# Optimization experiments

Measured on AMD Instinct MI355X. Metric: run time of the kernel, lower is better.

Reference implementation:

```python
import jax, jax.numpy as jnp
import numpy as np

HEADS = 4
DIM_HEAD = 32
DIM = HEADS * DIM_HEAD  # 128
B, H, W, C = 32, 64, 64, 128
LN_EPS = 1e-5


def setup_inputs() -> dict:
    key = jax.random.key(0)
    k0, k1, k2, k3, k4 = jax.random.split(key, 5)
    x = jax.random.normal(k0, (B, H, W, C), dtype=jnp.float32)
    # 1x1 convs are pointwise dense layers over channels
    w_qkv = jax.random.normal(k1, (C, DIM * 3), dtype=jnp.float32) * (1.0 / np.sqrt(C))
    w_out = jax.random.normal(k2, (DIM, C), dtype=jnp.float32) * (1.0 / np.sqrt(DIM))
    b_out = jax.random.normal(k3, (C,), dtype=jnp.float32) * 0.01
    ln_scale = jnp.ones((C,), dtype=jnp.float32)
    return {"x": x, "w_qkv": w_qkv, "w_out": w_out, "b_out": b_out, "ln_scale": ln_scale}


def reference(x, w_qkv, w_out, b_out, ln_scale):
    b, h, w, c = x.shape
    n = h * w
    # qkv projection (1x1 conv, no bias)
    qkv = jnp.einsum('bhwc,cf->bhwf', x, w_qkv)  # [B,H,W,3*DIM]
    q, k, v = jnp.split(qkv, 3, axis=-1)
    # rearrange 'b x y (h d) -> b (x y) h d'
    q = q.reshape(b, n, HEADS, DIM_HEAD)
    k = k.reshape(b, n, HEADS, DIM_HEAD)
    v = v.reshape(b, n, HEADS, DIM_HEAD)
    q = jax.nn.softmax(q, axis=-1) * (1.0 / np.sqrt(DIM_HEAD))
    k = jax.nn.softmax(k, axis=1)  # softmax over spatial positions
    v = v * (1.0 / n)
    # per-head context: [B, heads, d, e]
    context = jnp.einsum('bnhd,bnhe->bhde', k, v)
    # out: 'b h d e, b n h d -> b h e n', then rearrange 'b h e (x y) -> b x y (h e)'
    out = jnp.einsum('bhde,bnhd->bnhe', context, q)  # [B, n, heads, e]
    out = out.reshape(b, h, w, DIM)  # channel order = (h e), matching rearrange
    # output 1x1 conv (with bias)
    out = jnp.einsum('bhwd,dc->bhwc', out, w_out) + b_out
    # LayerNorm over channels, eps=1e-5, no bias
    mu = jnp.mean(out, axis=-1, keepdims=True)
    var = jnp.mean(jnp.square(out - mu), axis=-1, keepdims=True)
    out = (out - mu) * jax.lax.rsqrt(var + LN_EPS) * ln_scale
    return out
```

## Files before the change

### kernel.cpp

```cpp
#include <hip/hip_runtime.h>
#include <hip/hip_bf16.h>

typedef __attribute__((ext_vector_type(4))) float f32x4;
typedef __attribute__((ext_vector_type(8))) short bf16x8;
typedef __attribute__((ext_vector_type(8))) unsigned short u16x8;

#define OFF_QS    0ull
#define OFF_EK    33554432ull
#define OFF_VV    67108864ull
#define OFF_PCTX  100663296ull
#define OFF_PSE   109051904ull
#define OFF_CTXG  109314048ull
#define OFF_WQT   109576192ull
#define OFF_WOT   109674496ull

static __device__ __forceinline__ unsigned short f2bf(float f) {
  unsigned int u = __builtin_bit_cast(unsigned int, f);
  return (unsigned short)((u + 0x7fffu + ((u >> 16) & 1u)) >> 16);
}
static __device__ __forceinline__ float bf2f(unsigned short v) {
  return __builtin_bit_cast(float, (unsigned int)v << 16);
}

__global__ __launch_bounds__(256) void k_prep(const float* __restrict__ wqkv,
                                              const float* __restrict__ wout,
                                              unsigned short* __restrict__ wqT,
                                              unsigned short* __restrict__ woT) {
  int idx = blockIdx.x * 256 + threadIdx.x;
  if (idx < 49152) {
    int f = idx >> 7, k = idx & 127;
    wqT[idx] = f2bf(wqkv[k * 384 + f]);
  } else {
    int j = idx - 49152;
    int c = j >> 7, k = j & 127;
    woT[j] = f2bf(wout[k * 128 + c]);
  }
}

__global__ __launch_bounds__(512, 4) void k_qkv(const float* __restrict__ x,
                                                const unsigned short* __restrict__ wqT,
                                                unsigned short* __restrict__ qs,
                                                unsigned short* __restrict__ ekh,
                                                unsigned short* __restrict__ vvh) {
  extern __shared__ char lds[];
  char* lds_w = lds;
  char* lds_a = lds + 32768;

  const int tid = threadIdx.x;
  const int tile = blockIdx.x;
  const int sec = blockIdx.y;
  const long rowbase = (long)tile * 128;

  {
    const int4* src = (const int4*)wqT + sec * 2048;
#pragma unroll
    for (int i = 0; i < 4; i++) {
      int u = tid + i * 512;
      ((int4*)lds_w)[u ^ ((u >> 4) & 7)] = src[u];
    }
  }
  {
    const f32x4* src = (const f32x4*)(x + rowbase * 128);
#pragma unroll
    for (int i = 0; i < 8; i++) {
      int u = tid + i * 512;
      f32x4 val = src[u];
      ushort4 bq;
      bq.x = f2bf(val.x); bq.y = f2bf(val.y); bq.z = f2bf(val.z); bq.w = f2bf(val.w);
      int ba = (u * 8) ^ (((u >> 5) & 7) << 4);
      *(ushort4*)(lds_a + ba) = bq;
    }
  }
  __syncthreads();

  const int lane = tid & 63, g = lane >> 4, c = lane & 15;
  const int wave = tid >> 6;
  const int wm = wave >> 2, wf = wave & 3;

  f32x4 acc[4][2];
#pragma unroll
  for (int mt = 0; mt < 4; mt++) { acc[mt][0] = (f32x4){0.f,0.f,0.f,0.f}; acc[mt][1] = (f32x4){0.f,0.f,0.f,0.f}; }

#pragma unroll
  for (int kk = 0; kk < 4; kk++) {
    const int koff = (kk * 32 + g * 8) * 2;
    bf16x8 af[4], bfrag[2];
#pragma unroll
    for (int mt = 0; mt < 4; mt++) {
      int row = wm * 64 + mt * 16 + c;
      af[mt] = *(const bf16x8*)(lds_a + ((row * 256 + koff) ^ ((row & 7) << 4)));
    }
#pragma unroll
    for (int ft = 0; ft < 2; ft++) {
      int frow = wf * 32 + ft * 16 + c;
      bfrag[ft] = *(const bf16x8*)(lds_w + ((frow * 256 + koff) ^ ((frow & 7) << 4)));
    }
#pragma unroll
    for (int mt = 0; mt < 4; mt++)
#pragma unroll
      for (int ft = 0; ft < 2; ft++)
        acc[mt][ft] = __builtin_amdgcn_mfma_f32_16x16x32_bf16(af[mt], bfrag[ft], acc[mt][ft], 0, 0, 0);
  }
  __syncthreads();

  const float RS32 = 0.17677669529663687f;
  const int sc = wf * 32;
#pragma unroll
  for (int mt = 0; mt < 4; mt++) {
    f32x4 a0 = acc[mt][0], a1 = acc[mt][1];
    int row0 = wm * 64 + mt * 16 + g * 4;
    if (sec == 0) {
#pragma unroll
      for (int r = 0; r < 4; r++) {
        float e0 = __expf(a0[r]), e1 = __expf(a1[r]);
        float s = e0 + e1;
        s += __shfl_xor(s, 1); s += __shfl_xor(s, 2);
        s += __shfl_xor(s, 4); s += __shfl_xor(s, 8);
        float inv = RS32 / s;
        int row = row0 + r;
        *(unsigned short*)(lds + ((row * 256 + (sc + c) * 2)      ^ ((row & 7) << 4))) = f2bf(e0 * inv);
        *(unsigned short*)(lds + ((row * 256 + (sc + c + 16) * 2) ^ ((row & 7) << 4))) = f2bf(e1 * inv);
      }
    } else if (sec == 1) {
#pragma unroll
      for (int r = 0; r < 4; r++) {
        int row = row0 + r;
        *(unsigned short*)(lds + ((row * 256 + (sc + c) * 2)      ^ ((row & 7) << 4))) = f2bf(__expf(a0[r]));
        *(unsigned short*)(lds + ((row * 256 + (sc + c + 16) * 2) ^ ((row & 7) << 4))) = f2bf(__expf(a1[r]));
      }
    } else {
#pragma unroll
      for (int r = 0; r < 4; r++) {
        int row = row0 + r;
        *(unsigned short*)(lds + ((row * 256 + (sc + c) * 2)      ^ ((row & 7) << 4))) = f2bf(a0[r]);
        *(unsigned short*)(lds + ((row * 256 + (sc + c + 16) * 2) ^ ((row & 7) << 4))) = f2bf(a1[r]);
      }
    }
  }
  __syncthreads();

  if (sec == 0) {
    const long off16 = (long)tile * 2048;
#pragma unroll
    for (int i = 0; i < 4; i++) {
      int u = tid + i * 512;
      int row = u >> 4;
      int4 v = *(const int4*)(lds + ((u * 16) ^ ((row & 7) << 4)));
      ((int4*)qs)[off16 + u] = v;
    }
  } else {
    unsigned short* dsth = (sec == 1) ? ekh : vvh;
#pragma unroll
    for (int i = 0; i < 4; i++) {
      int u = tid + i * 512;
      int row = u >> 4, col16 = u & 15;
      int h = col16 >> 2, q4 = col16 & 3;
      int4 v = *(const int4*)(lds + ((u * 16) ^ ((row & 7) << 4)));
      long di = ((long)h * 131072 + tile * 128 + row) * 4 + q4;
      ((int4*)dsth)[di] = v;
    }
  }
}

__global__ __launch_bounds__(256, 4) void k_ctx(const unsigned short* __restrict__ ekh,
                                                const unsigned short* __restrict__ vvh,
                                                float* __restrict__ pctx,
                                                float* __restrict__ pse) {
  extern __shared__ char lds[];

  const int tid = threadIdx.x;
  const int h = blockIdx.x & 3, quarter = blockIdx.x >> 2, b = blockIdx.y;
  const int wave = tid >> 6, lane = tid & 63, g = lane >> 4, c = lane & 15;
  const long nbase = (long)b * 4096 + quarter * 1024;

  f32x4 acc[2][2];
#pragma unroll
  for (int dt = 0; dt < 2; dt++) { acc[dt][0] = (f32x4){0.f,0.f,0.f,0.f}; acc[dt][1] = (f32x4){0.f,0.f,0.f,0.f}; }
  float se[2] = {0.f, 0.f};

  for (int sci = 0; sci < 4; sci++) {
    const long n0 = nbase + sci * 256;
    const uint4* esrc = (const uint4*)(ekh + ((long)h * 131072 + n0 + tid) * 32);
    const uint4* vsrc = (const uint4*)(vvh + ((long)h * 131072 + n0 + tid) * 32);
    uint4 ev[4], vq[4];
#pragma unroll
    for (int i = 0; i < 4; i++) { ev[i] = esrc[i]; vq[i] = vsrc[i]; }

    if (sci > 0) __syncthreads();

#pragma unroll
    for (int i = 0; i < 4; i++) {
      u16x8 es = __builtin_bit_cast(u16x8, ev[i]);
      u16x8 vs = __builtin_bit_cast(u16x8, vq[i]);
#pragma unroll
      for (int j = 0; j < 8; j++) {
        int d = i * 8 + j;
        int ba = (d * 512 + tid * 2) ^ ((d & 7) << 4);
        *(unsigned short*)(lds + ba)         = es[j];
        *(unsigned short*)(lds + 16384 + ba) = vs[j];
      }
    }
    __syncthreads();

#pragma unroll
    for (int ks = 0; ks < 2; ks++) {
      const int noff = (wave * 64 + ks * 32 + g * 8) * 2;
      bf16x8 afr[2], bfr[2];
#pragma unroll
      for (int dt = 0; dt < 2; dt++) {
        int row = dt * 16 + c;
        afr[dt] = *(const bf16x8*)(lds + ((row * 512 + noff) ^ ((row & 7) << 4)));
      }
#pragma unroll
      for (int et = 0; et < 2; et++) {
        int row = et * 16 + c;
        bfr[et] = *(const bf16x8*)(lds + 16384 + ((row * 512 + noff) ^ ((row & 7) << 4)));
      }
#pragma unroll
      for (int dt = 0; dt < 2; dt++)
#pragma unroll
        for (int j = 0; j < 8; j++)
          se[dt] += bf2f((unsigned short)afr[dt][j]);
#pragma unroll
      for (int dt = 0; dt < 2; dt++)
#pragma unroll
        for (int et = 0; et < 2; et++)
          acc[dt][et] = __builtin_amdgcn_mfma_f32_16x16x32_bf16(afr[dt], bfr[et], acc[dt][et], 0, 0, 0);
    }
  }

  const int p = quarter * 4 + wave;
  const long pb = ((long)p * 128 + b * 4 + h) * 1024;
#pragma unroll
  for (int dt = 0; dt < 2; dt++)
#pragma unroll
    for (int et = 0; et < 2; et++)
#pragma unroll
      for (int r = 0; r < 4; r++)
        pctx[pb + (dt * 16 + g * 4 + r) * 32 + et * 16 + c] = acc[dt][et][r];

#pragma unroll
  for (int dt = 0; dt < 2; dt++) {
    se[dt] += __shfl_xor(se[dt], 16);
    se[dt] += __shfl_xor(se[dt], 32);
  }
  if (lane < 16) {
#pragma unroll
    for (int dt = 0; dt < 2; dt++)
      pse[((long)p * 128 + b * 4 + h) * 32 + dt * 16 + c] = se[dt];
  }
}

__global__ __launch_bounds__(256) void k_ctxred(const float* __restrict__ pctx,
                                                const float* __restrict__ pse,
                                                unsigned short* __restrict__ ctxg) {
  int idx = blockIdx.x * 256 + threadIdx.x;
  int de = idx & 1023, d = de >> 5, bh = idx >> 10;
  float s = 0.f, sume = 0.f;
#pragma unroll
  for (int ch = 0; ch < 16; ch++) {
    s    += pctx[(ch * 128 + bh) * 1024 + de];
    sume += pse[(ch * 128 + bh) * 32 + d];
  }
  ctxg[idx] = f2bf(s / (sume * 4096.0f));
}

__global__ __launch_bounds__(512, 2) void k_out(const unsigned short* __restrict__ qs,
                                                const unsigned short* __restrict__ ctxg,
                                                const unsigned short* __restrict__ woT,
                                                const float* __restrict__ bout,
                                                const float* __restrict__ lnsc,
                                                float* __restrict__ out) {
  extern __shared__ char lds[];
  char* lds_wo = lds;
  char* lds_at = lds + 32768;
  unsigned short* lds_cx = (unsigned short*)(lds + 65536);
  float* lds_bias  = (float*)(lds + 73728);
  float* lds_scale = (float*)(lds + 74240);

  const int tid = threadIdx.x;
  const long rowbase = (long)blockIdx.x * 128;
  const int b = blockIdx.x >> 5;

  {
    const int4* src = (const int4*)woT;
    int4* dst = (int4*)lds_wo;
#pragma unroll
    for (int i = 0; i < 4; i++) {
      int u = tid + i * 512;
      dst[u ^ ((u >> 4) & 7)] = src[u];
    }
  }
  {
    const unsigned int* src = (const unsigned int*)(ctxg + (long)b * 4096);
#pragma unroll
    for (int i = 0; i < 4; i++) {
      int u = tid + i * 512;
      unsigned int w = src[u];
      int j = u * 2;
      int e = j & 31, d = (j >> 5) & 31, h = j >> 10;
      lds_cx[(h * 32 + e) * 32 + d]     = (unsigned short)(w & 0xffffu);
      lds_cx[(h * 32 + e + 1) * 32 + d] = (unsigned short)(w >> 16);
    }
  }
  if (tid < 128) { lds_bias[tid] = bout[tid]; lds_scale[tid] = lnsc[tid]; }
  __syncthreads();

  const int lane = tid & 63, g = lane >> 4, c = lane & 15;
  const int wave = tid >> 6;

  f32x4 acc1[4][2];
#pragma unroll
  for (int h = 0; h < 4; h++) { acc1[h][0] = (f32x4){0.f,0.f,0.f,0.f}; acc1[h][1] = (f32x4){0.f,0.f,0.f,0.f}; }
  const unsigned short* qrow = qs + (rowbase + wave * 16 + c) * 128;
#pragma unroll
  for (int h = 0; h < 4; h++) {
    bf16x8 a = *(const bf16x8*)(qrow + h * 32 + g * 8);
#pragma unroll
    for (int et = 0; et < 2; et++) {
      bf16x8 bq = *(const bf16x8*)(lds_cx + (h * 32 + et * 16 + c) * 32 + g * 8);
      acc1[h][et] = __builtin_amdgcn_mfma_f32_16x16x32_bf16(a, bq, acc1[h][et], 0, 0, 0);
    }
  }
  {
    int rowl = wave * 16 + g * 4;
#pragma unroll
    for (int h = 0; h < 4; h++)
#pragma unroll
      for (int et = 0; et < 2; et++) {
        int col = (2 * h + et) * 16 + c;
#pragma unroll
        for (int r = 0; r < 4; r++) {
          int row = rowl + r;
          int ba = (row * 256 + col * 2) ^ ((row & 7) << 4);
          *(unsigned short*)(lds_at + ba) = f2bf(acc1[h][et][r]);
        }
      }
  }
  __syncthreads();

  f32x4 acc2[8];
#pragma unroll
  for (int ct = 0; ct < 8; ct++) acc2[ct] = (f32x4){0.f,0.f,0.f,0.f};
#pragma unroll
  for (int kk = 0; kk < 4; kk++) {
    int koff = (kk * 32 + g * 8) * 2;
    int arow = wave * 16 + c;
    bf16x8 a = *(const bf16x8*)(lds_at + ((arow * 256 + koff) ^ ((arow & 7) << 4)));
#pragma unroll
    for (int ct = 0; ct < 8; ct++) {
      int wrow = ct * 16 + c;
      bf16x8 bw = *(const bf16x8*)(lds_wo + ((wrow * 256 + koff) ^ ((wrow & 7) << 4)));
      acc2[ct] = __builtin_amdgcn_mfma_f32_16x16x32_bf16(a, bw, acc2[ct], 0, 0, 0);
    }
  }

  float biasv[8], scalev[8];
#pragma unroll
  for (int ct = 0; ct < 8; ct++) { biasv[ct] = lds_bias[ct * 16 + c]; scalev[ct] = lds_scale[ct * 16 + c]; }
#pragma unroll
  for (int ct = 0; ct < 8; ct++)
#pragma unroll
    for (int r = 0; r < 4; r++)
      acc2[ct][r] += biasv[ct];

#pragma unroll
  for (int r = 0; r < 4; r++) {
    float s = 0.f, ss = 0.f;
#pragma unroll
    for (int ct = 0; ct < 8; ct++) { float v = acc2[ct][r]; s += v; ss += v * v; }
    s  += __shfl_xor(s, 1);  s  += __shfl_xor(s, 2);  s  += __shfl_xor(s, 4);  s  += __shfl_xor(s, 8);
    ss += __shfl_xor(ss, 1); ss += __shfl_xor(ss, 2); ss += __shfl_xor(ss, 4); ss += __shfl_xor(ss, 8);
    float mu = s * 0.0078125f;
    float var = ss * 0.0078125f - mu * mu;
    float rstd = rsqrtf(var + 1e-5f);
#pragma unroll
    for (int ct = 0; ct < 8; ct++)
      acc2[ct][r] = (acc2[ct][r] - mu) * rstd * scalev[ct];
  }

#pragma unroll
  for (int half = 0; half < 2; half++) {
    __syncthreads();
    if ((wave >> 2) == half) {
      int rl0 = (wave & 3) * 16 + g * 4;
#pragma unroll
      for (int ct = 0; ct < 8; ct++)
#pragma unroll
        for (int r = 0; r < 4; r++) {
          int rl = rl0 + r;
          *(float*)(lds_at + ((rl * 512 + (ct * 16 + c) * 4) ^ ((rl & 7) << 4))) = acc2[ct][r];
        }
    }
    __syncthreads();
    {
      const long base = (rowbase + half * 64) * 32;
#pragma unroll
      for (int i = 0; i < 4; i++) {
        int u = tid + i * 512;
        int row = u >> 5;
        int4 v = *(const int4*)(lds_at + ((u * 16) ^ ((row & 7) << 4)));
        ((int4*)out)[base + u] = v;
      }
    }
  }
}

extern "C" void kernel_launch(void* const* d_in, const int* in_sizes, int n_in,
                              void* d_out, int out_size, void* d_ws, size_t ws_size,
                              hipStream_t stream) {
  (void)in_sizes; (void)n_in; (void)out_size; (void)ws_size;
  const float* x     = (const float*)d_in[0];
  const float* wqkv  = (const float*)d_in[1];
  const float* wout  = (const float*)d_in[2];
  const float* bo    = (const float*)d_in[3];
  const float* lnsc  = (const float*)d_in[4];
  float* out = (float*)d_out;

  char* ws = (char*)d_ws;
  unsigned short* qs   = (unsigned short*)(ws + OFF_QS);
  unsigned short* ekh  = (unsigned short*)(ws + OFF_EK);
  unsigned short* vvh  = (unsigned short*)(ws + OFF_VV);
  float*          pctx = (float*)(ws + OFF_PCTX);
  float*          pse  = (float*)(ws + OFF_PSE);
  unsigned short* ctxg = (unsigned short*)(ws + OFF_CTXG);
  unsigned short* wqT  = (unsigned short*)(ws + OFF_WQT);
  unsigned short* woT  = (unsigned short*)(ws + OFF_WOT);

  k_prep<<<dim3(256), dim3(256), 0, stream>>>(wqkv, wout, wqT, woT);
  k_qkv<<<dim3(1024, 3), dim3(512), 65536, stream>>>(x, wqT, qs, ekh, vvh);
  k_ctx<<<dim3(16, 32), dim3(256), 32768, stream>>>(ekh, vvh, pctx, pse);
  k_ctxred<<<dim3(512), dim3(256), 0, stream>>>(pctx, pse, ctxg);
  k_out<<<dim3(1024), dim3(512), 74752, stream>>>(qs, ctxg, woT, bo, lnsc, out);
}
```

Before: 195.2 us.

## Halve qkv row tile and read output weights directly from global memory

The qkv projection kernel now processes 64 rows per block instead of 128, with a new wave-to-tile mapping. Each wave does 1x4 MFMA tiles instead of 4x2, the grid doubles, LDS per block shrinks and the occupancy hint rises. The output kernel no longer stages the transposed out-projection weights in LDS and reads B fragments straight from global/L2, cutting LDS use to allow more resident blocks. In exchange, the weight tile is loaded twice as often in k_qkv, and k_out issues many more global loads in its inner MFMA loop.

```diff
diff --git a/kernel.cpp b/kernel.cpp
--- a/kernel.cpp
+++ b/kernel.cpp
@@ -37,7 +37,7 @@
   }
 }
 
-__global__ __launch_bounds__(512, 4) void k_qkv(const float* __restrict__ x,
+__global__ __launch_bounds__(512, 6) void k_qkv(const float* __restrict__ x,
                                                 const unsigned short* __restrict__ wqT,
                                                 unsigned short* __restrict__ qs,
                                                 unsigned short* __restrict__ ekh,
@@ -49,7 +49,7 @@
   const int tid = threadIdx.x;
   const int tile = blockIdx.x;
   const int sec = blockIdx.y;
-  const long rowbase = (long)tile * 128;
+  const long rowbase = (long)tile * 64;
 
   {
     const int4* src = (const int4*)wqT + sec * 2048;
@@ -62,7 +62,7 @@
   {
     const f32x4* src = (const f32x4*)(x + rowbase * 128);
 #pragma unroll
-    for (int i = 0; i < 8; i++) {
+    for (int i = 0; i < 4; i++) {
       int u = tid + i * 512;
       f32x4 val = src[u];
       ushort4 bq;
@@ -75,40 +75,32 @@
 
   const int lane = tid & 63, g = lane >> 4, c = lane & 15;
   const int wave = tid >> 6;
-  const int wm = wave >> 2, wf = wave & 3;
-
-  f32x4 acc[4][2];
-#pragma unroll
-  for (int mt = 0; mt < 4; mt++) { acc[mt][0] = (f32x4){0.f,0.f,0.f,0.f}; acc[mt][1] = (f32x4){0.f,0.f,0.f,0.f}; }
+  const int wm = wave >> 1, wf = wave & 1;
+
+  f32x4 acc[4];
+#pragma unroll
+  for (int ft = 0; ft < 4; ft++) acc[ft] = (f32x4){0.f, 0.f, 0.f, 0.f};
 
 #pragma unroll
   for (int kk = 0; kk < 4; kk++) {
     const int koff = (kk * 32 + g * 8) * 2;
-    bf16x8 af[4], bfrag[2];
-#pragma unroll
-    for (int mt = 0; mt < 4; mt++) {
-      int row = wm * 64 + mt * 16 + c;
-      af[mt] = *(const bf16x8*)(lds_a + ((row * 256 + koff) ^ ((row & 7) << 4)));
-    }
-#pragma unroll
-    for (int ft = 0; ft < 2; ft++) {
-      int frow = wf * 32 + ft * 16 + c;
-      bfrag[ft] = *(const bf16x8*)(lds_w + ((frow * 256 + koff) ^ ((frow & 7) << 4)));
-    }
-#pragma unroll
-    for (int mt = 0; mt < 4; mt++)
-#pragma unroll
-      for (int ft = 0; ft < 2; ft++)
-        acc[mt][ft] = __builtin_amdgcn_mfma_f32_16x16x32_bf16(af[mt], bfrag[ft], acc[mt][ft], 0, 0, 0);
+    const int arow = wm * 16 + c;
+    bf16x8 af = *(const bf16x8*)(lds_a + ((arow * 256 + koff) ^ ((arow & 7) << 4)));
+#pragma unroll
+    for (int ft = 0; ft < 4; ft++) {
+      int frow = wf * 64 + ft * 16 + c;
+      bf16x8 bfrag = *(const bf16x8*)(lds_w + ((frow * 256 + koff) ^ ((frow & 7) << 4)));
+      acc[ft] = __builtin_amdgcn_mfma_f32_16x16x32_bf16(af, bfrag, acc[ft], 0, 0, 0);
+    }
   }
   __syncthreads();
 
   const float RS32 = 0.17677669529663687f;
-  const int sc = wf * 32;
-#pragma unroll
-  for (int mt = 0; mt < 4; mt++) {
-    f32x4 a0 = acc[mt][0], a1 = acc[mt][1];
-    int row0 = wm * 64 + mt * 16 + g * 4;
+#pragma unroll
+  for (int j = 0; j < 2; j++) {
+    const int sc = wf * 64 + j * 32;
+    f32x4 a0 = acc[2 * j], a1 = acc[2 * j + 1];
+    const int row0 = wm * 16 + g * 4;
     if (sec == 0) {
 #pragma unroll
       for (int r = 0; r < 4; r++) {
@@ -140,9 +132,9 @@
   __syncthreads();
 
   if (sec == 0) {
-    const long off16 = (long)tile * 2048;
-#pragma unroll
-    for (int i = 0; i < 4; i++) {
+    const long off16 = (long)tile * 1024;
+#pragma unroll
+    for (int i = 0; i < 2; i++) {
       int u = tid + i * 512;
       int row = u >> 4;
       int4 v = *(const int4*)(lds + ((u * 16) ^ ((row & 7) << 4)));
@@ -151,12 +143,12 @@
   } else {
     unsigned short* dsth = (sec == 1) ? ekh : vvh;
 #pragma unroll
-    for (int i = 0; i < 4; i++) {
+    for (int i = 0; i < 2; i++) {
       int u = tid + i * 512;
       int row = u >> 4, col16 = u & 15;
       int h = col16 >> 2, q4 = col16 & 3;
       int4 v = *(const int4*)(lds + ((u * 16) ^ ((row & 7) << 4)));
-      long di = ((long)h * 131072 + tile * 128 + row) * 4 + q4;
+      long di = ((long)h * 131072 + tile * 64 + row) * 4 + q4;
       ((int4*)dsth)[di] = v;
     }
   }
@@ -272,25 +264,15 @@
                                                 const float* __restrict__ lnsc,
                                                 float* __restrict__ out) {
   extern __shared__ char lds[];
-  char* lds_wo = lds;
-  char* lds_at = lds + 32768;
-  unsigned short* lds_cx = (unsigned short*)(lds + 65536);
-  float* lds_bias  = (float*)(lds + 73728);
-  float* lds_scale = (float*)(lds + 74240);
+  char* lds_at = lds;
+  unsigned short* lds_cx = (unsigned short*)(lds + 32768);
+  float* lds_bias  = (float*)(lds + 40960);
+  float* lds_scale = (float*)(lds + 41472);
 
   const int tid = threadIdx.x;
   const long rowbase = (long)blockIdx.x * 128;
   const int b = blockIdx.x >> 5;
 
-  {
-    const int4* src = (const int4*)woT;
-    int4* dst = (int4*)lds_wo;
-#pragma unroll
-    for (int i = 0; i < 4; i++) {
-      int u = tid + i * 512;
-      dst[u ^ ((u >> 4) & 7)] = src[u];
-    }
-  }
   {
     const unsigned int* src = (const unsigned int*)(ctxg + (long)b * 4096);
 #pragma unroll
@@ -350,7 +332,7 @@
 #pragma unroll
     for (int ct = 0; ct < 8; ct++) {
       int wrow = ct * 16 + c;
-      bf16x8 bw = *(const bf16x8*)(lds_wo + ((wrow * 256 + koff) ^ ((wrow & 7) << 4)));
+      bf16x8 bw = *(const bf16x8*)(woT + wrow * 128 + kk * 32 + g * 8);
       acc2[ct] = __builtin_amdgcn_mfma_f32_16x16x32_bf16(a, bw, acc2[ct], 0, 0, 0);
     }
   }
@@ -428,8 +410,8 @@
   unsigned short* woT  = (unsigned short*)(ws + OFF_WOT);
 
   k_prep<<<dim3(256), dim3(256), 0, stream>>>(wqkv, wout, wqT, woT);
-  k_qkv<<<dim3(1024, 3), dim3(512), 65536, stream>>>(x, wqT, qs, ekh, vvh);
+  k_qkv<<<dim3(2048, 3), dim3(512), 49152, stream>>>(x, wqT, qs, ekh, vvh);
   k_ctx<<<dim3(16, 32), dim3(256), 32768, stream>>>(ekh, vvh, pctx, pse);
   k_ctxred<<<dim3(512), dim3(256), 0, stream>>>(pctx, pse, ctxg);
-  k_out<<<dim3(1024), dim3(512), 74752, stream>>>(qs, ctxg, woT, bo, lnsc, out);
-}
+  k_out<<<dim3(1024), dim3(512), 41984, stream>>>(qs, ctxg, woT, bo, lnsc, out);
+}
```

Result: slower. 209.8 us (+7.5%).
